# Kernel optimization log

Hardware: AMD Instinct MI355X
Metric: run time of the kernel (lower is better)

The kernel has to match this reference:

```python
import jax, jax.numpy as jnp
import numpy as np

B, H, W = 16, 32, 64
HID, VOCAB, ENC_C, EMB = 256, 5000, 1024, 256


def _conv3x3(x, w, b):
    # x: [B,C,H,W], w: [O,I,3,3]
    y = jax.lax.conv_general_dilated(x, w, (1, 1), 'SAME',
                                     dimension_numbers=('NCHW', 'OIHW', 'NCHW'))
    return y + b[None, :, None, None]


def _gru(x, h, w_ih, w_hh, b_ih, b_hh):
    # torch GRUCell: gates ordered r, z, n
    gi = x @ w_ih.T + b_ih
    gh = h @ w_hh.T + b_hh
    ir, iz, inn = jnp.split(gi, 3, axis=1)
    hr, hz, hn = jnp.split(gh, 3, axis=1)
    r = jax.nn.sigmoid(ir + hr)
    z = jax.nn.sigmoid(iz + hz)
    n = jnp.tanh(inn + r * hn)
    return (1.0 - z) * n + z * h


def setup_inputs() -> dict:
    key = jax.random.key(0)
    ks = jax.random.split(key, 48)
    g = lambda i, shape, s=0.02: jax.random.normal(ks[i], shape, jnp.float32) * s
    inp = {
        'input_a': jax.random.randint(ks[0], (B,), 0, VOCAB),
        'input_hidden': jax.random.normal(ks[1], (B, 1, HID), jnp.float32),
        'encoder_outputs': jax.random.normal(ks[2], (B, ENC_C, H, W), jnp.float32),
        'attention_sum': jnp.zeros((B, 1, H, W), jnp.float32),
        'decoder_attention': jnp.zeros((B, 1, H, W), jnp.float32),
        'h_mask': jax.random.randint(ks[3], (B,), 1, H + 1),
        'w_mask': jax.random.randint(ks[4], (B,), 1, W + 1),
        'feature_w': W, 'feature_h': H, 'batch_size': B, 'gpu': 0,
        # parameters
        'emb_w': g(5, (VOCAB, EMB)),
        'gru1_w_ih': g(6, (3 * HID, EMB)), 'gru1_w_hh': g(7, (3 * HID, HID)),
        'gru1_b_ih': jnp.zeros((3 * HID,)), 'gru1_b_hh': jnp.zeros((3 * HID,)),
        'fc1_w': g(8, (256, HID)), 'fc1_b': jnp.zeros((256,)),
        'gru2_w_ih': g(9, (3 * HID, ENC_C)), 'gru2_w_hh': g(10, (3 * HID, HID)),
        'gru2_b_ih': jnp.zeros((3 * HID,)), 'gru2_b_hh': jnp.zeros((3 * HID,)),
        'out_w': g(11, (VOCAB, 128)), 'out_b': jnp.zeros((VOCAB,)),
        'emb2_w': g(12, (128, 256)), 'emb2_b': jnp.zeros((128,)),
        'conv1_w': g(13, (1, 1, 3, 3)), 'conv1_b': jnp.zeros((1,)),
        'convtan_w': g(14, (256, 256, 3, 3)), 'convtan_b': jnp.zeros((256,)),
        'fc2_w': g(15, (128, HID)), 'fc2_b': jnp.zeros((128,)),
        'ua_w': g(16, (256, ENC_C)), 'ua_b': jnp.zeros((256,)),
        'uf_w': g(17, (256, 1)), 'uf_b': jnp.zeros((256,)),
        'v_w': g(18, (1, 256)), 'v_b': jnp.zeros((1,)),
        'wc_w': g(19, (128, ENC_C)), 'wc_b': jnp.zeros((128,)),
        'bn1_g': jnp.ones((256,)), 'bn1_b': jnp.zeros((256,)),
        'bn1_rm': jnp.zeros((256,)), 'bn1_rv': jnp.ones((256,)),
    }
    return inp


def reference(input_a, input_hidden, encoder_outputs, feature_w, attention_sum,
              decoder_attention, feature_h, batch_size, h_mask, w_mask, gpu,
              emb_w, gru1_w_ih, gru1_w_hh, gru1_b_ih, gru1_b_hh, fc1_w, fc1_b,
              gru2_w_ih, gru2_w_hh, gru2_b_ih, gru2_b_hh, out_w, out_b,
              emb2_w, emb2_b, conv1_w, conv1_b, convtan_w, convtan_b,
              fc2_w, fc2_b, ua_w, ua_b, uf_w, uf_b, v_w, v_b, wc_w, wc_b,
              bn1_g, bn1_b, bn1_rm, bn1_rv):
    # vectorized mask construction (replaces per-batch python loop)
    mask = ((jnp.arange(feature_h)[None, :, None] < h_mask[:, None, None]) &
            (jnp.arange(feature_w)[None, None, :] < w_mask[:, None, None])
            ).astype(jnp.float32)  # [B,H,W]

    emb = emb_w[input_a]                                   # [B,256] (dropout=eval id)
    h0 = input_hidden.reshape(batch_size, HID)
    st = _gru(emb, h0, gru1_w_ih, gru1_w_hh, gru1_b_ih, gru1_b_hh)  # [B,HID]
    hidden1 = (st @ fc1_w.T + fc1_b)[:, None, None, :]     # [B,1,1,256]

    enc_t = jnp.transpose(encoder_outputs, (0, 2, 3, 1))   # [B,H,W,1024]
    dec_att = _conv3x3(decoder_attention, conv1_w, conv1_b)
    att_sum = attention_sum + dec_att                      # [B,1,H,W]
    att_t = jnp.transpose(att_sum, (0, 2, 3, 1))           # [B,H,W,1]

    enc1 = enc_t @ ua_w.T + ua_b                           # [B,H,W,256]
    att1 = att_t @ uf_w.T + uf_b                           # [B,H,W,256]
    et = hidden1 + enc1 + att1

    et_c = jnp.transpose(et, (0, 3, 1, 2))                 # [B,256,H,W]
    et_c = _conv3x3(et_c, convtan_w, convtan_b)
    et_c = et_c * mask[:, None]
    inv_std = (bn1_g / jnp.sqrt(bn1_rv + 1e-5))[None, :, None, None]
    et_c = (et_c - bn1_rm[None, :, None, None]) * inv_std + bn1_b[None, :, None, None]
    et_c = jnp.tanh(et_c)
    et_hw = jnp.transpose(et_c, (0, 2, 3, 1))              # [B,H,W,256]

    e = (et_hw @ v_w.T + v_b)[..., 0]                      # [B,H,W]
    e_exp = jnp.exp(e) * mask
    e_sum = e_exp.sum((1, 2))                              # [B]
    alpha = e_exp / (e_sum[:, None, None] + 1e-8)
    alpha4 = alpha[:, None]                                # [B,1,H,W]

    ct = (alpha4 * encoder_outputs).sum((2, 3))            # [B,1024]
    h2 = _gru(ct, st, gru2_w_ih, gru2_w_hh, gru2_b_ih, gru2_b_hh)
    hidden_next = h2[:, None, :]                           # [B,1,HID]

    pre = (h2 @ fc2_w.T + fc2_b) + (emb @ emb2_w.T + emb2_b) + (ct @ wc_w.T + wc_b)
    output = jax.nn.log_softmax(pre @ out_w.T + out_b, axis=1)[:, None, :]  # [B,1,V]
    return (output, hidden_next, alpha4, att_sum)
```

## Files before the change

kernel.cpp:

```cpp
#include <hip/hip_runtime.h>
#include <hip/hip_bf16.h>

#define HH 32
#define WW 64
#define HWSZ 2048
#define ENC 1024
#define VOCAB 5000

typedef __attribute__((ext_vector_type(8))) short short8;
typedef __attribute__((ext_vector_type(4))) short short4v;
typedef __attribute__((ext_vector_type(4))) float f32x4;

__device__ __forceinline__ float sigm(float x) { return 1.0f / (1.0f + expf(-x)); }

__device__ __forceinline__ unsigned short f2bf(float x) {
    unsigned u = __float_as_uint(x);
    unsigned r = (u + 0x7fff + ((u >> 16) & 1)) >> 16;
    return (unsigned short)r;
}

template <int NI>
__device__ __forceinline__ float dotk(const float* __restrict__ w,
                                      const float* __restrict__ x, int l) {
    float s = 0.f;
    #pragma unroll
    for (int i = 0; i < NI; ++i) {
        f32x4 wv = *(const f32x4*)(w + i * 64 + l * 4);
        f32x4 xv = *(const f32x4*)(x + i * 64 + l * 4);
        s += wv.x * xv.x + wv.y * xv.y + wv.z * xv.z + wv.w * xv.w;
    }
    return s;
}
__device__ __forceinline__ float red16(float s) {
    s += __shfl_xor(s, 1, 64);
    s += __shfl_xor(s, 2, 64);
    s += __shfl_xor(s, 4, 64);
    s += __shfl_xor(s, 8, 64);
    return s;
}

__global__ __launch_bounds__(256) void k_prep(
    const float* __restrict__ ua_w, unsigned short* __restrict__ ub,
    const float* __restrict__ cw, unsigned short* __restrict__ wr,
    const float* __restrict__ att_in, const float* __restrict__ dec,
    const float* __restrict__ c1w, const float* __restrict__ c1b,
    float* __restrict__ out_attsum,
    const float* __restrict__ wb, const float* __restrict__ g,
    const float* __restrict__ bb, const float* __restrict__ rm,
    const float* __restrict__ rv, float* __restrict__ cs, float* __restrict__ csh,
    const int* __restrict__ input_a, const float* __restrict__ input_hidden,
    const float* __restrict__ emb_w,
    const float* __restrict__ w_ih, const float* __restrict__ w_hh,
    const float* __restrict__ b_ih, const float* __restrict__ b_hh,
    float* __restrict__ gi, float* __restrict__ gh,
    float* __restrict__ e_zero)
{
    int blk = blockIdx.x, t = threadIdx.x;
    if (blk < 1024) {
        int idx = blk * 256 + t;
        ub[idx] = f2bf(ua_w[idx]);
    } else if (blk < 1280) {
        int idx = (blk - 1024) * 256 + t;
        const float* p = cw + (size_t)idx * 9;
        #pragma unroll
        for (int k = 0; k < 9; ++k) wr[k * 65536 + idx] = f2bf(p[k]);
    } else if (blk < 1408) {
        int idx = (blk - 1280) * 256 + t;
        int b = idx >> 11, hw = idx & 2047;
        int h = hw >> 6, w = hw & 63;
        float s = c1b[0];
        #pragma unroll
        for (int dy = 0; dy < 3; ++dy) {
            int hh = h + dy - 1;
            if ((unsigned)hh < (unsigned)HH) {
                #pragma unroll
                for (int dx = 0; dx < 3; ++dx) {
                    int wi = w + dx - 1;
                    if ((unsigned)wi < (unsigned)WW)
                        s += dec[b * HWSZ + hh * WW + wi] * c1w[dy * 3 + dx];
                }
            }
        }
        out_attsum[idx] = att_in[idx] + s;
    } else if (blk == 1408) {
        int c = t;
        float s = g[c] * rsqrtf(rv[c] + 1e-5f);
        cs[c] = s;
        csh[c] = (wb[c] - rm[c]) * s + bb[c];
    } else if (blk < 2177) {
        int gid = (blk - 1409) * 256 + t;
        int o = gid >> 4, l = gid & 15;
        int j = o >> 4, b = o & 15;
        int ia = input_a[b];
        float si = dotk<4>(w_ih + (size_t)j * 256, emb_w + (size_t)ia * 256, l);
        float sh = dotk<4>(w_hh + (size_t)j * 256, input_hidden + b * 256, l);
        si = red16(si); sh = red16(sh);
        if (l == 0) {
            gi[j * 16 + b] = si + b_ih[j];
            gh[j * 16 + b] = sh + b_hh[j];
        }
    } else {
        e_zero[(blk - 2177) * 256 + t] = 0.f;
    }
}

__global__ __launch_bounds__(256) void k_frontbc(
    const int* __restrict__ input_a, const float* __restrict__ emb_w,
    const float* __restrict__ input_hidden,
    const float* __restrict__ gi, const float* __restrict__ gh,
    const float* __restrict__ fc1_w, const float* __restrict__ fc1_b,
    const float* __restrict__ ua_b, const float* __restrict__ uf_b,
    float* __restrict__ st, float* __restrict__ embv, float* __restrict__ addc)
{
    __shared__ float st_s[256];
    int b = blockIdx.x, i = threadIdx.x;
    float r = sigm(gi[i * 16 + b] + gh[i * 16 + b]);
    float z = sigm(gi[(256 + i) * 16 + b] + gh[(256 + i) * 16 + b]);
    float n = tanhf(gi[(512 + i) * 16 + b] + r * gh[(512 + i) * 16 + b]);
    float h0 = input_hidden[b * 256 + i];
    float v = (1.f - z) * n + z * h0;
    st_s[i] = v;
    st[b * 256 + i] = v;
    embv[b * 256 + i] = emb_w[(size_t)input_a[b] * 256 + i];
    __syncthreads();
    int c = i;
    const float* w = fc1_w + (size_t)c * 256;
    float acc = 0.f;
    for (int k = 0; k < 256; ++k) acc += st_s[k] * w[k];
    addc[b * 256 + c] = acc + fc1_b[c] + ua_b[c] + uf_b[c];
}

__global__ __launch_bounds__(256) void k_et(
    const float* __restrict__ enc, const unsigned short* __restrict__ ua_bf,
    const float* __restrict__ addc, const float* __restrict__ uf_w,
    const float* __restrict__ attsum, unsigned short* __restrict__ et)
{
    __shared__ unsigned short Bs[32 * 40];
    int t = threadIdx.x;
    int hw0 = blockIdx.x * 32, b = blockIdx.y;
    int wv = t >> 6;
    int l15 = t & 15, quad = (t >> 4) & 3;
    f32x4 acc[4][2];
    #pragma unroll
    for (int i = 0; i < 4; ++i)
        #pragma unroll
        for (int j = 0; j < 2; ++j) acc[i][j] = (f32x4)0.f;

    int sww = t & 31;
    int sgrp = t >> 5;
    int sp = ((sgrp >> 1) + (sww >> 3)) & 3;
    const float* encb = enc + (size_t)b * ENC * HWSZ + hw0 + sww;

    float pf[4];
    {
        const float* ep = encb + (size_t)(sgrp * 4) * HWSZ;
        #pragma unroll
        for (int i = 0; i < 4; ++i) pf[i] = ep[(size_t)i * HWSZ];
    }
    for (int k0 = 0; k0 < ENC; k0 += 32) {
        short4v v;
        #pragma unroll
        for (int i = 0; i < 4; ++i) v[i] = (short)f2bf(pf[i]);
        __syncthreads();
        *(short4v*)(Bs + sww * 40 + sp * 8 + (sgrp & 1) * 4) = v;
        __syncthreads();
        if (k0 + 32 < ENC) {
            const float* ep = encb + (size_t)(k0 + 32 + sgrp * 4) * HWSZ;
            #pragma unroll
            for (int i = 0; i < 4; ++i) pf[i] = ep[(size_t)i * HWSZ];
        }
        short8 af[4], bfr[2];
        #pragma unroll
        for (int mt = 0; mt < 4; ++mt)
            af[mt] = *(const short8*)(ua_bf +
                (size_t)(wv * 64 + mt * 16 + l15) * ENC + k0 + quad * 8);
        #pragma unroll
        for (int nt = 0; nt < 2; ++nt) {
            int n = nt * 16 + l15;
            int slot = (quad + (n >> 3)) & 3;
            bfr[nt] = *(const short8*)(Bs + n * 40 + slot * 8);
        }
        #pragma unroll
        for (int mt = 0; mt < 4; ++mt)
            #pragma unroll
            for (int nt = 0; nt < 2; ++nt)
                acc[mt][nt] = __builtin_amdgcn_mfma_f32_16x16x32_bf16(
                    af[mt], bfr[nt], acc[mt][nt], 0, 0, 0);
    }
    float at[2];
    #pragma unroll
    for (int nt = 0; nt < 2; ++nt) at[nt] = attsum[b * HWSZ + hw0 + nt * 16 + l15];
    #pragma unroll
    for (int mt = 0; mt < 4; ++mt) {
        int cb = wv * 64 + mt * 16 + quad * 4;
        float ad[4], uw[4];
        #pragma unroll
        for (int r = 0; r < 4; ++r) { ad[r] = addc[b * 256 + cb + r]; uw[r] = uf_w[cb + r]; }
        #pragma unroll
        for (int nt = 0; nt < 2; ++nt) {
            ushort4 pk;
            pk.x = f2bf(acc[mt][nt][0] + ad[0] + at[nt] * uw[0]);
            pk.y = f2bf(acc[mt][nt][1] + ad[1] + at[nt] * uw[1]);
            pk.z = f2bf(acc[mt][nt][2] + ad[2] + at[nt] * uw[2]);
            pk.w = f2bf(acc[mt][nt][3] + ad[3] + at[nt] * uw[3]);
            *(ushort4*)(et + (size_t)(b * HWSZ + hw0 + nt * 16 + l15) * 256 + cb) = pk;
        }
    }
}

__global__ __launch_bounds__(256) void k_conv(
    const unsigned short* __restrict__ et, const unsigned short* __restrict__ wr,
    const float* __restrict__ cs, const float* __restrict__ csh,
    const float* __restrict__ v_w, float* __restrict__ e_out)
{
    __shared__ unsigned short Ls[66 * 264];
    __shared__ float red[64][17];
    int t = threadIdx.x;
    int h = blockIdx.x, c0 = blockIdx.y * 128, b = blockIdx.z;
    int wv = t >> 6, l15 = t & 15, quad = (t >> 4) & 3;
    f32x4 acc[2][4];
    #pragma unroll
    for (int i = 0; i < 2; ++i)
        #pragma unroll
        for (int j = 0; j < 4; ++j) acc[i][j] = (f32x4)0.f;

    for (int dy = 0; dy < 3; ++dy) {
        int hr = h + dy - 1;
        if ((unsigned)hr >= (unsigned)HH) continue;
        __syncthreads();
        const unsigned short* rowp = et + (size_t)(b * HH + hr) * WW * 256;
        for (int idx = t; idx < 2112; idx += 256) {
            int p = idx >> 5, s = idx & 31;
            short8 v;
            if (p == 0 || p == 65) v = (short8)0;
            else v = *(const short8*)(rowp + (p - 1) * 256 + s * 8);
            *(short8*)(Ls + p * 264 + s * 8) = v;
        }
        __syncthreads();
        for (int dx = 0; dx < 3; ++dx) {
            int tap = dy * 3 + dx;
            const unsigned short* wrt = wr + (size_t)tap * 65536;
            #pragma unroll
            for (int kc = 0; kc < 8; ++kc) {
                short8 af[2], bfr[4];
                #pragma unroll
                for (int mt = 0; mt < 2; ++mt)
                    af[mt] = *(const short8*)(wrt +
                        (size_t)(c0 + wv * 32 + mt * 16 + l15) * 256 + kc * 32 + quad * 8);
                #pragma unroll
                for (int nt = 0; nt < 4; ++nt) {
                    int wrow = nt * 16 + l15 + dx;
                    bfr[nt] = *(const short8*)(Ls + wrow * 264 + kc * 32 + quad * 8);
                }
                #pragma unroll
                for (int mt = 0; mt < 2; ++mt)
                    #pragma unroll
                    for (int nt = 0; nt < 4; ++nt)
                        acc[mt][nt] = __builtin_amdgcn_mfma_f32_16x16x32_bf16(
                            af[mt], bfr[nt], acc[mt][nt], 0, 0, 0);
            }
        }
    }
    float p[4] = {0.f, 0.f, 0.f, 0.f};
    #pragma unroll
    for (int mt = 0; mt < 2; ++mt) {
        int cb = c0 + wv * 32 + mt * 16 + quad * 4;
        #pragma unroll
        for (int r = 0; r < 4; ++r) {
            float sc = cs[cb + r], sh = csh[cb + r], vw = v_w[cb + r];
            #pragma unroll
            for (int nt = 0; nt < 4; ++nt) {
                float x = acc[mt][nt][r] * sc + sh;
                p[nt] += tanhf(x) * vw;
            }
        }
    }
    __syncthreads();
    #pragma unroll
    for (int nt = 0; nt < 4; ++nt) red[nt * 16 + l15][wv * 4 + quad] = p[nt];
    __syncthreads();
    if (t < 64) {
        float s = 0.f;
        #pragma unroll
        for (int i = 0; i < 16; ++i) s += red[t][i];
        atomicAdd(&e_out[(b * HH + h) * WW + t], s);
    }
}

__global__ __launch_bounds__(256) void k_ctalpha(
    const float* __restrict__ enc, const float* __restrict__ e_acc,
    const float* __restrict__ v_b,
    const int* __restrict__ h_mask, const int* __restrict__ w_mask,
    float* __restrict__ alpha_out, float* __restrict__ ct)
{
    __shared__ float a_s[HWSZ];
    __shared__ float rbuf[4];
    int b = blockIdx.y, cg = blockIdx.x, t = threadIdx.x;
    int hm = h_mask[b], wm = w_mask[b];
    float vb = v_b[0];
    float vals[8];
    float psum = 0.f;
    #pragma unroll
    for (int u = 0; u < 8; ++u) {
        int s = u * 256 + t;
        int h = s >> 6, w = s & 63;
        float e = e_acc[b * HWSZ + s] + vb;
        float ex = (h < hm && w < wm) ? expf(e) : 0.f;
        vals[u] = ex;
        psum += ex;
    }
    for (int off = 1; off < 64; off <<= 1) psum += __shfl_xor(psum, off, 64);
    if ((t & 63) == 0) rbuf[t >> 6] = psum;
    __syncthreads();
    float inv = 1.f / (rbuf[0] + rbuf[1] + rbuf[2] + rbuf[3] + 1e-8f);
    #pragma unroll
    for (int u = 0; u < 8; ++u) {
        int s = u * 256 + t;
        float a = vals[u] * inv;
        a_s[s] = a;
        if (cg == 0) alpha_out[b * HWSZ + s] = a;
    }
    __syncthreads();
    int wave = t >> 6, lane = t & 63;
    int c = cg * 4 + wave;
    const float* ep = enc + ((size_t)(b * ENC + c)) * HWSZ;
    float s = 0.f;
    for (int i = lane; i < HWSZ; i += 64) s += ep[i] * a_s[i];
    for (int off = 32; off; off >>= 1) s += __shfl_down(s, off, 64);
    if (lane == 0) ct[b * ENC + c] = s;
}

__global__ __launch_bounds__(256) void k_gru2a(
    const float* __restrict__ ct, const float* __restrict__ st,
    const float* __restrict__ w_ih, const float* __restrict__ w_hh,
    const float* __restrict__ b_ih, const float* __restrict__ b_hh,
    float* __restrict__ gi, float* __restrict__ gh)
{
    int gid = blockIdx.x * 256 + threadIdx.x;
    int o = gid >> 4, l = gid & 15;
    int j = o >> 4, b = o & 15;
    float si = dotk<16>(w_ih + (size_t)j * ENC, ct + b * ENC, l);
    float sh = dotk<4>(w_hh + (size_t)j * 256, st + b * 256, l);
    si = red16(si); sh = red16(sh);
    if (l == 0) {
        gi[j * 16 + b] = si + b_ih[j];
        gh[j * 16 + b] = sh + b_hh[j];
    }
}

__global__ __launch_bounds__(256) void k_gates2(
    const float* __restrict__ st, const float* __restrict__ gi,
    const float* __restrict__ gh, float* __restrict__ h2,
    float* __restrict__ out_hidden)
{
    int b = blockIdx.x, i = threadIdx.x;
    float r = sigm(gi[i * 16 + b] + gh[i * 16 + b]);
    float z = sigm(gi[(256 + i) * 16 + b] + gh[(256 + i) * 16 + b]);
    float n = tanhf(gi[(512 + i) * 16 + b] + r * gh[(512 + i) * 16 + b]);
    float v = (1.f - z) * n + z * st[b * 256 + i];
    h2[b * 256 + i] = v;
    out_hidden[b * 256 + i] = v;
}

__global__ __launch_bounds__(256) void k_pre(
    const float* __restrict__ h2, const float* __restrict__ emb,
    const float* __restrict__ ct,
    const float* __restrict__ fc2_w, const float* __restrict__ fc2_b,
    const float* __restrict__ emb2_w, const float* __restrict__ emb2_b,
    const float* __restrict__ wc_w, const float* __restrict__ wc_b,
    float* __restrict__ pre)
{
    int gid = blockIdx.x * 256 + threadIdx.x;
    int o = gid >> 4, l = gid & 15;
    int j = o >> 4, b = o & 15;
    float s = dotk<4>(fc2_w + (size_t)j * 256, h2 + b * 256, l)
            + dotk<4>(emb2_w + (size_t)j * 256, emb + b * 256, l)
            + dotk<16>(wc_w + (size_t)j * ENC, ct + b * ENC, l);
    s = red16(s);
    if (l == 0) pre[b * 128 + j] = s + fc2_b[j] + emb2_b[j] + wc_b[j];
}

__global__ __launch_bounds__(256) void k_logits(
    const float* __restrict__ pre, const float* __restrict__ out_w,
    const float* __restrict__ out_b, float* __restrict__ logits)
{
    int gid = blockIdx.x * 256 + threadIdx.x;
    int o = gid >> 4, l = gid & 15;
    int j = o >> 4, b = o & 15;
    float s = dotk<2>(out_w + (size_t)j * 128, pre + b * 128, l);
    s = red16(s);
    if (l == 0) logits[b * VOCAB + j] = s + out_b[j];
}

__global__ __launch_bounds__(256) void k_lsm(
    const float* __restrict__ logits, float* __restrict__ out)
{
    __shared__ float buf[VOCAB];
    __shared__ float rbuf[4];
    int b = blockIdx.x, t = threadIdx.x;
    float mx = -1e30f;
    for (int s = t; s < VOCAB; s += 256) {
        float v = logits[b * VOCAB + s];
        buf[s] = v;
        mx = fmaxf(mx, v);
    }
    for (int off = 1; off < 64; off <<= 1) mx = fmaxf(mx, __shfl_xor(mx, off, 64));
    if ((t & 63) == 0) rbuf[t >> 6] = mx;
    __syncthreads();
    mx = fmaxf(fmaxf(rbuf[0], rbuf[1]), fmaxf(rbuf[2], rbuf[3]));
    __syncthreads();
    float se = 0.f;
    for (int s = t; s < VOCAB; s += 256) se += expf(buf[s] - mx);
    for (int off = 1; off < 64; off <<= 1) se += __shfl_xor(se, off, 64);
    if ((t & 63) == 0) rbuf[t >> 6] = se;
    __syncthreads();
    float lse = mx + logf(rbuf[0] + rbuf[1] + rbuf[2] + rbuf[3]);
    for (int s = t; s < VOCAB; s += 256) out[b * VOCAB + s] = buf[s] - lse;
}

extern "C" void kernel_launch(void* const* d_in, const int* in_sizes, int n_in,
                              void* d_out, int out_size, void* d_ws, size_t ws_size,
                              hipStream_t stream)
{
    const int*   input_a      = (const int*)d_in[0];
    const float* input_hidden = (const float*)d_in[1];
    const float* enc          = (const float*)d_in[2];
    const float* att_in       = (const float*)d_in[3];
    const float* dec_att      = (const float*)d_in[4];
    const int*   h_mask       = (const int*)d_in[5];
    const int*   w_mask       = (const int*)d_in[6];
    const float* emb_w        = (const float*)d_in[11];
    const float* g1_wih       = (const float*)d_in[12];
    const float* g1_whh       = (const float*)d_in[13];
    const float* g1_bih       = (const float*)d_in[14];
    const float* g1_bhh       = (const float*)d_in[15];
    const float* fc1_w        = (const float*)d_in[16];
    const float* fc1_b        = (const float*)d_in[17];
    const float* g2_wih       = (const float*)d_in[18];
    const float* g2_whh       = (const float*)d_in[19];
    const float* g2_bih       = (const float*)d_in[20];
    const float* g2_bhh       = (const float*)d_in[21];
    const float* out_w        = (const float*)d_in[22];
    const float* out_b        = (const float*)d_in[23];
    const float* emb2_w       = (const float*)d_in[24];
    const float* emb2_b       = (const float*)d_in[25];
    const float* c1w          = (const float*)d_in[26];
    const float* c1b          = (const float*)d_in[27];
    const float* ctw          = (const float*)d_in[28];
    const float* ctb          = (const float*)d_in[29];
    const float* fc2_w        = (const float*)d_in[30];
    const float* fc2_b        = (const float*)d_in[31];
    const float* ua_w         = (const float*)d_in[32];
    const float* ua_b         = (const float*)d_in[33];
    const float* uf_w         = (const float*)d_in[34];
    const float* uf_b         = (const float*)d_in[35];
    const float* v_w          = (const float*)d_in[36];
    const float* v_b          = (const float*)d_in[37];
    const float* wc_w         = (const float*)d_in[38];
    const float* wc_b         = (const float*)d_in[39];
    const float* bn_g         = (const float*)d_in[40];
    const float* bn_b         = (const float*)d_in[41];
    const float* bn_rm        = (const float*)d_in[42];
    const float* bn_rv        = (const float*)d_in[43];

    float* out        = (float*)d_out;
    float* out_logits = out;
    float* out_hidden = out + 80000;
    float* out_alpha  = out + 84096;
    float* out_attsum = out + 116864;

    char* ws = (char*)d_ws;
    unsigned short* et_t  = (unsigned short*)ws;
    unsigned short* ua_bf = (unsigned short*)(ws + 16777216);
    unsigned short* w_r   = (unsigned short*)(ws + 17301504);
    float* f      = (float*)(ws + 18481152);
    float* st     = f;
    float* embv   = f + 4096;
    float* addc   = f + 8192;
    float* e_ws   = f + 12288;
    float* ct     = f + 45056;
    float* h2     = f + 61440;
    float* pre    = f + 65536;
    float* logits = f + 67584;
    float* gi1    = f + 147584;
    float* gh1    = f + 159872;
    float* gi2    = f + 172160;
    float* gh2    = f + 184448;
    float* cs     = f + 196736;
    float* csh    = f + 196992;

    k_prep<<<2305, 256, 0, stream>>>(ua_w, ua_bf, ctw, w_r,
                                     att_in, dec_att, c1w, c1b, out_attsum,
                                     ctb, bn_g, bn_b, bn_rm, bn_rv, cs, csh,
                                     input_a, input_hidden, emb_w,
                                     g1_wih, g1_whh, g1_bih, g1_bhh, gi1, gh1,
                                     e_ws);
    k_frontbc<<<16, 256, 0, stream>>>(input_a, emb_w, input_hidden, gi1, gh1,
                                      fc1_w, fc1_b, ua_b, uf_b, st, embv, addc);

    k_et<<<dim3(64, 16), 256, 0, stream>>>(enc, ua_bf, addc, uf_w, out_attsum, et_t);
    k_conv<<<dim3(32, 2, 16), 256, 0, stream>>>(et_t, w_r, cs, csh, v_w, e_ws);

    k_ctalpha<<<dim3(256, 16), 256, 0, stream>>>(enc, e_ws, v_b, h_mask, w_mask,
                                                 out_alpha, ct);
    k_gru2a<<<768, 256, 0, stream>>>(ct, st, g2_wih, g2_whh, g2_bih, g2_bhh, gi2, gh2);
    k_gates2<<<16, 256, 0, stream>>>(st, gi2, gh2, h2, out_hidden);
    k_pre<<<128, 256, 0, stream>>>(h2, embv, ct, fc2_w, fc2_b, emb2_w, emb2_b,
                                   wc_w, wc_b, pre);
    k_logits<<<5000, 256, 0, stream>>>(pre, out_w, out_b, logits);
    k_lsm<<<16, 256, 0, stream>>>(logits, out_logits);
}
```

Before: 488.1 us.

## Stage ua weights in LDS via direct global-to-LDS loads with XOR swizzle

The k_et GEMM kernel now copies the bf16 ua weight tile into shared memory each K step, using global_load_lds when the builtin is available, instead of having each wave read A fragments straight from global memory. The K step grows from 32 to 64 with two MFMA sub-steps, and both the A and B tiles use an XOR swizzle to avoid LDS bank conflicts. The goal is coalesced weight loads and fewer barriers per K. In exchange the kernel needs about 36 KB of LDS per block, which may reduce occupancy.

```diff
diff --git a/kernel.cpp b/kernel.cpp
--- a/kernel.cpp
+++ b/kernel.cpp
@@ -11,6 +11,12 @@
 typedef __attribute__((ext_vector_type(4))) short short4v;
 typedef __attribute__((ext_vector_type(4))) float f32x4;
 
+#if defined(__has_builtin)
+#if __has_builtin(__builtin_amdgcn_global_load_lds)
+#define HAVE_GLD_LDS 1
+#endif
+#endif
+
 __device__ __forceinline__ float sigm(float x) { return 1.0f / (1.0f + expf(-x)); }
 
 __device__ __forceinline__ unsigned short f2bf(float x) {
@@ -18,6 +24,15 @@
     unsigned r = (u + 0x7fff + ((u >> 16) & 1)) >> 16;
     return (unsigned short)r;
 }
+
+#ifdef HAVE_GLD_LDS
+__device__ __forceinline__ void gld_lds16(const unsigned short* g, unsigned short* l) {
+    __builtin_amdgcn_global_load_lds(
+        (const __attribute__((address_space(1))) void*)g,
+        (__attribute__((address_space(3))) void*)l,
+        16, 0, 0);
+}
+#endif
 
 template <int NI>
 __device__ __forceinline__ float dotk(const float* __restrict__ w,
@@ -135,57 +150,75 @@
     const float* __restrict__ addc, const float* __restrict__ uf_w,
     const float* __restrict__ attsum, unsigned short* __restrict__ et)
 {
-    __shared__ unsigned short Bs[32 * 40];
+    __shared__ __align__(16) unsigned short As[256 * 64];
+    __shared__ __align__(16) unsigned short Bs[32 * 64];
     int t = threadIdx.x;
     int hw0 = blockIdx.x * 32, b = blockIdx.y;
     int wv = t >> 6;
     int l15 = t & 15, quad = (t >> 4) & 3;
+    int xb = l15 & 7;
     f32x4 acc[4][2];
     #pragma unroll
     for (int i = 0; i < 4; ++i)
         #pragma unroll
         for (int j = 0; j < 2; ++j) acc[i][j] = (f32x4)0.f;
 
-    int sww = t & 31;
-    int sgrp = t >> 5;
-    int sp = ((sgrp >> 1) + (sww >> 3)) & 3;
-    const float* encb = enc + (size_t)b * ENC * HWSZ + hw0 + sww;
-
-    float pf[4];
+    int p = t & 31, g3 = t >> 5;
+    const float* encb = enc + (size_t)b * ENC * HWSZ + hw0 + p;
+
+    float pfv[8];
     {
-        const float* ep = encb + (size_t)(sgrp * 4) * HWSZ;
-        #pragma unroll
-        for (int i = 0; i < 4; ++i) pf[i] = ep[(size_t)i * HWSZ];
-    }
-    for (int k0 = 0; k0 < ENC; k0 += 32) {
-        short4v v;
-        #pragma unroll
-        for (int i = 0; i < 4; ++i) v[i] = (short)f2bf(pf[i]);
+        const float* ep = encb + (size_t)(g3 * 8) * HWSZ;
+        #pragma unroll
+        for (int j = 0; j < 8; ++j) pfv[j] = ep[(size_t)j * HWSZ];
+    }
+
+    for (int k0 = 0; k0 < ENC; k0 += 64) {
+        short8 bv;
+        #pragma unroll
+        for (int j = 0; j < 8; ++j) bv[j] = (short)f2bf(pfv[j]);
+        if (k0 + 64 < ENC) {
+            const float* ep = encb + (size_t)(k0 + 64 + g3 * 8) * HWSZ;
+            #pragma unroll
+            for (int j = 0; j < 8; ++j) pfv[j] = ep[(size_t)j * HWSZ];
+        }
         __syncthreads();
-        *(short4v*)(Bs + sww * 40 + sp * 8 + (sgrp & 1) * 4) = v;
+
+        #pragma unroll
+        for (int i = 0; i < 8; ++i) {
+            int s = t + 256 * i;
+            int c = s >> 3, kq = s & 7;
+            const unsigned short* src =
+                ua_bf + (size_t)c * ENC + k0 + ((kq ^ (c & 7)) << 3);
+#ifdef HAVE_GLD_LDS
+            gld_lds16(src, As + (size_t)(wv * 64 + 256 * i) * 8);
+#else
+            *(uint4*)(As + (size_t)s * 8) = *(const uint4*)src;
+#endif
+        }
+        *(short8*)(Bs + p * 64 + ((g3 ^ (p & 7)) << 3)) = bv;
         __syncthreads();
-        if (k0 + 32 < ENC) {
-            const float* ep = encb + (size_t)(k0 + 32 + sgrp * 4) * HWSZ;
+
+        #pragma unroll
+        for (int kk = 0; kk < 2; ++kk) {
+            short8 af[4], bfr[2];
             #pragma unroll
-            for (int i = 0; i < 4; ++i) pf[i] = ep[(size_t)i * HWSZ];
-        }
-        short8 af[4], bfr[2];
-        #pragma unroll
-        for (int mt = 0; mt < 4; ++mt)
-            af[mt] = *(const short8*)(ua_bf +
-                (size_t)(wv * 64 + mt * 16 + l15) * ENC + k0 + quad * 8);
-        #pragma unroll
-        for (int nt = 0; nt < 2; ++nt) {
-            int n = nt * 16 + l15;
-            int slot = (quad + (n >> 3)) & 3;
-            bfr[nt] = *(const short8*)(Bs + n * 40 + slot * 8);
-        }
-        #pragma unroll
-        for (int mt = 0; mt < 4; ++mt)
+            for (int mt = 0; mt < 4; ++mt) {
+                int c = wv * 64 + mt * 16 + l15;
+                af[mt] = *(const short8*)(As + c * 64 + (((kk * 4 + quad) ^ xb) << 3));
+            }
             #pragma unroll
-            for (int nt = 0; nt < 2; ++nt)
-                acc[mt][nt] = __builtin_amdgcn_mfma_f32_16x16x32_bf16(
-                    af[mt], bfr[nt], acc[mt][nt], 0, 0, 0);
+            for (int nt = 0; nt < 2; ++nt) {
+                int n = nt * 16 + l15;
+                bfr[nt] = *(const short8*)(Bs + n * 64 + (((kk * 4 + quad) ^ xb) << 3));
+            }
+            #pragma unroll
+            for (int mt = 0; mt < 4; ++mt)
+                #pragma unroll
+                for (int nt = 0; nt < 2; ++nt)
+                    acc[mt][nt] = __builtin_amdgcn_mfma_f32_16x16x32_bf16(
+                        af[mt], bfr[nt], acc[mt][nt], 0, 0, 0);
+        }
     }
     float at[2];
     #pragma unroll
```

New measurement: 452.0 us. 7.4% less time.
